# Kernel tuning notes

Measured on AMD Instinct MI355X. Metric: run time of the kernel, lower is better.

Reference implementation:

```python
import math
import jax, jax.numpy as jnp
import numpy as np

SEQ_LEN = 512
NUM_HEADS = 16
HEAD_DIM = 64  # hidden_size // num_heads
MAX_REL = 127


def _relative_positions_embeddings(length, depth, max_relative_position=MAX_REL):
    """Sinusoidal table gathered by clipped relative distance -> [L, L, depth]."""
    vocab = 2 * max_relative_position + 1
    pos = np.arange(vocab, dtype=np.float64)[:, None]
    i = np.arange(depth // 2, dtype=np.float64)[None, :]
    angle = pos / np.power(10000.0, 2.0 * i / depth)
    table = np.zeros((vocab, depth), dtype=np.float64)
    table[:, 0::2] = np.sin(angle)
    table[:, 1::2] = np.cos(angle)
    r = np.arange(length)
    dist = np.clip(r[None, :] - r[:, None], -max_relative_position, max_relative_position)
    final = dist + max_relative_position  # [L, L] indices into vocab
    return jnp.asarray(table[final], dtype=jnp.float32)  # [L, L, depth]

_REL_EMB = _relative_positions_embeddings(SEQ_LEN, HEAD_DIM)


def setup_inputs() -> dict:
    key = jax.random.key(0)
    ks = jax.random.split(key, 4)
    B, S, H = 8, SEQ_LEN, NUM_HEADS * HEAD_DIM
    scale = 1.0 / math.sqrt(H)
    return {
        "hidden_states": jax.random.normal(ks[0], (B, S, H), dtype=jnp.float32),
        "attention_mask": jnp.zeros((B, 1, 1, S), dtype=jnp.float32),
        "Wq": jax.random.normal(ks[1], (H, H), dtype=jnp.float32) * scale,
        "bq": jnp.zeros((H,), dtype=jnp.float32),
        "Wk": jax.random.normal(ks[2], (H, H), dtype=jnp.float32) * scale,
        "bk": jnp.zeros((H,), dtype=jnp.float32),
        "Wv": jax.random.normal(ks[3], (H, H), dtype=jnp.float32) * scale,
        "bv": jnp.zeros((H,), dtype=jnp.float32),
    }


def reference(hidden_states, attention_mask, Wq, bq, Wk, bk, Wv, bv):
    B, S, _ = hidden_states.shape
    H, D = NUM_HEADS, HEAD_DIM

    def split_heads(x):  # [B,S,H*D] -> [B,H,S,D]
        return x.reshape(B, S, H, D).transpose(0, 2, 1, 3)

    q = split_heads(hidden_states @ Wq.T + bq)
    k = split_heads(hidden_states @ Wk.T + bk)
    v = split_heads(hidden_states @ Wv.T + bv)

    rel = _REL_EMB[:S, :S, :]  # [S, S, D]

    scores = jnp.einsum("bhqd,bhkd->bhqk", q, k)
    scores = scores + jnp.einsum("bhqd,qkd->bhqk", q, rel)
    scores = scores / math.sqrt(D) + attention_mask

    probs = jax.nn.softmax(scores, axis=-1)  # dropout prob = 0.0 (eval)

    ctx = jnp.einsum("bhqk,bhkd->bhqd", probs, v)
    ctx = ctx + jnp.einsum("bhqk,qkd->bhqd", probs, rel)

    context_layer = ctx.transpose(0, 2, 1, 3).reshape(B, S, H * D)
    return context_layer, scores
```

## Files before the change

kernel.cpp:

```cpp
#include <hip/hip_runtime.h>
#include <hip/hip_bf16.h>

typedef __attribute__((ext_vector_type(4))) float f32x4;
typedef __attribute__((ext_vector_type(8))) short bf16x8;

#define NB 8
#define NS 512
#define NH 16
#define ND 64
#define HID 1024
#define NBH (NB*NH)
#define NROWS (NB*NS)

static __device__ __forceinline__ ushort f2bf(float x){
    union{float f; unsigned u;} a; a.f = x;
    unsigned r = a.u + 0x7fffu + ((a.u >> 16) & 1u);
    return (ushort)(r >> 16);
}
static __device__ __forceinline__ float bf2f(ushort x){
    union{unsigned u; float f;} a; a.u = ((unsigned)x) << 16;
    return a.f;
}

__global__ void build_tables(ushort* __restrict__ tab, ushort* __restrict__ tabT){
    int t = blockIdx.x * blockDim.x + threadIdx.x;
    if (t >= 256 * 64) return;
    int p = t >> 6, d = t & 63;
    float val = 0.f;
    if (p < 255){
        int i = d >> 1;
        float angle = (float)p / powf(10000.f, (float)i / 32.f);
        val = (d & 1) ? cosf(angle) : sinf(angle);
    }
    ushort b = f2bf(val);
    tab[p * 64 + d]  = b;
    tabT[d * 256 + p] = b;
}

__global__ void cvt_bf16(const float* __restrict__ src, ushort* __restrict__ dst, int n4){
    int i = blockIdx.x * blockDim.x + threadIdx.x;
    if (i >= n4) return;
    float4 v = reinterpret_cast<const float4*>(src)[i];
    ushort4 o;
    o.x = f2bf(v.x); o.y = f2bf(v.y); o.z = f2bf(v.z); o.w = f2bf(v.w);
    reinterpret_cast<ushort4*>(dst)[i] = o;
}

__global__ void cvt_bf16_w3(const float* __restrict__ w0, const float* __restrict__ w1,
                            const float* __restrict__ w2, ushort* __restrict__ o0,
                            ushort* __restrict__ o1, ushort* __restrict__ o2, int n4){
    int i = blockIdx.x * blockDim.x + threadIdx.x;
    if (i >= n4) return;
    const float* src = blockIdx.y == 0 ? w0 : (blockIdx.y == 1 ? w1 : w2);
    ushort* dst      = blockIdx.y == 0 ? o0 : (blockIdx.y == 1 ? o1 : o2);
    float4 v = reinterpret_cast<const float4*>(src)[i];
    ushort4 o;
    o.x = f2bf(v.x); o.y = f2bf(v.y); o.z = f2bf(v.z); o.w = f2bf(v.w);
    reinterpret_cast<ushort4*>(dst)[i] = o;
}

__global__ __launch_bounds__(256) void proj_gemm_qkv(
    const ushort* __restrict__ X,
    const ushort* __restrict__ Wqp, const ushort* __restrict__ Wkp, const ushort* __restrict__ Wvp,
    const float* __restrict__ bqp, const float* __restrict__ bkp, const float* __restrict__ bvp,
    ushort* __restrict__ outQ, ushort* __restrict__ outK, ushort* __restrict__ outV)
{
    __shared__ ushort lA[128][72];
    __shared__ ushort lB[128][72];
    int sel = blockIdx.x >> 3;
    const ushort* W   = sel == 0 ? Wqp : (sel == 1 ? Wkp : Wvp);
    const float* bias = sel == 0 ? bqp : (sel == 1 ? bkp : bvp);
    ushort* out       = sel == 0 ? outQ : (sel == 1 ? outK : outV);
    int n0 = (blockIdx.x & 7) * 128;
    int m0 = blockIdx.y * 128;
    int tid = threadIdx.x;
    int wave = tid >> 6, lane = tid & 63;
    int wr = (wave >> 1) * 64, wc = (wave & 1) * 64;
    int lrow = lane & 15, lk8 = (lane >> 4) * 8;

    f32x4 acc[4][4] = {};

    for (int k0 = 0; k0 < HID; k0 += 64){
        __syncthreads();
        #pragma unroll
        for (int i = 0; i < 4; ++i){
            int chunk = i * 256 + tid;
            int row = chunk >> 3, col = (chunk & 7) * 8;
            *reinterpret_cast<uint4*>(&lA[row][col]) =
                *reinterpret_cast<const uint4*>(&X[(size_t)(m0 + row) * HID + k0 + col]);
            *reinterpret_cast<uint4*>(&lB[row][col]) =
                *reinterpret_cast<const uint4*>(&W[(size_t)(n0 + row) * HID + k0 + col]);
        }
        __syncthreads();
        #pragma unroll
        for (int ks = 0; ks < 2; ++ks){
            bf16x8 af[4], bfr[4];
            #pragma unroll
            for (int m = 0; m < 4; ++m)
                af[m] = *reinterpret_cast<const bf16x8*>(&lA[wr + m*16 + lrow][ks*32 + lk8]);
            #pragma unroll
            for (int n = 0; n < 4; ++n)
                bfr[n] = *reinterpret_cast<const bf16x8*>(&lB[wc + n*16 + lrow][ks*32 + lk8]);
            #pragma unroll
            for (int m = 0; m < 4; ++m)
                #pragma unroll
                for (int n = 0; n < 4; ++n)
                    acc[m][n] = __builtin_amdgcn_mfma_f32_16x16x32_bf16(af[m], bfr[n], acc[m][n], 0, 0, 0);
        }
    }

    #pragma unroll
    for (int m = 0; m < 4; ++m){
        #pragma unroll
        for (int n = 0; n < 4; ++n){
            int col = n0 + wc + n*16 + lrow;
            float bv = bias[col];
            int h = col >> 6, d = col & 63;
            #pragma unroll
            for (int r = 0; r < 4; ++r){
                int mg = m0 + wr + m*16 + (lane >> 4)*4 + r;
                int b = mg >> 9, s = mg & 511;
                float val = acc[m][n][r] + bv;
                if (sel != 2)
                    out[(((size_t)(b*NH + h))*NS + s)*ND + d] = f2bf(val);
                else
                    out[(((size_t)(b*NH + h))*ND + d)*NS + s] = f2bf(val);
            }
        }
    }
}

__global__ __launch_bounds__(256) void fused_attn(
    const ushort* __restrict__ Qb, const ushort* __restrict__ Kb,
    const ushort* __restrict__ vT, const ushort* __restrict__ tab,
    const ushort* __restrict__ tabT, const float* __restrict__ mask,
    float* __restrict__ scores, float* __restrict__ ctx)
{
    __shared__ ushort pL[16][512];
    __shared__ ushort qq[16][256];
    __shared__ float  rsum[16][4];
    __shared__ float  rleft[16][4];
    __shared__ float  rright[16][4];
    ushort* pLf = &pL[0][0];
    ushort* qqf = &qq[0][0];
#define SWZ(row, col) ((col) ^ (((row)&7)<<3))

    const int bh = blockIdx.x;
    const int b = bh >> 4, h = bh & 15;
    const int q0 = blockIdx.y * 16;
    const int wave = threadIdx.x >> 6, lane = threadIdx.x & 63;
    const int lrow = lane & 15, g = lane >> 4, lk8 = g * 8;

    const ushort* Qh = Qb + (size_t)bh * NS * ND;
    const ushort* Kh = Kb + (size_t)bh * NS * ND;
    const int d = wave*16 + lrow;
    const ushort* vTh = vT + ((size_t)bh*ND + d)*NS;

    bf16x8 qf[2];
    #pragma unroll
    for (int ks = 0; ks < 2; ++ks)
        qf[ks] = *reinterpret_cast<const bf16x8*>(&Qh[(size_t)(q0 + lrow)*ND + ks*32 + lk8]);

    f32x4 acc[12];
    #pragma unroll
    for (int n = 0; n < 12; ++n) acc[n] = (f32x4){0.f, 0.f, 0.f, 0.f};

    #pragma unroll
    for (int n = 0; n < 12; ++n){
        const ushort* src = (n < 8) ? &Kh[(size_t)(wave*128 + n*16 + lrow)*ND]
                                    : &tab[(size_t)(wave*64 + (n-8)*16 + lrow)*ND];
        #pragma unroll
        for (int ks = 0; ks < 2; ++ks){
            bf16x8 kf = *reinterpret_cast<const bf16x8*>(&src[ks*32 + lk8]);
            acc[n] = __builtin_amdgcn_mfma_f32_16x16x32_bf16(kf, qf[ks], acc[n], 0, 0, 0);
        }
    }

    bf16x8 vpre[8];
    #pragma unroll
    for (int i = 0; i < 8; ++i)
        vpre[i] = *reinterpret_cast<const bf16x8*>(&vTh[i*64 + lk8]);

    #pragma unroll
    for (int n = 8; n < 12; ++n){
        ushort4 w;
        w.x = f2bf(acc[n][0]); w.y = f2bf(acc[n][1]);
        w.z = f2bf(acc[n][2]); w.w = f2bf(acc[n][3]);
        int col = wave*64 + (n-8)*16 + g*4;
        *reinterpret_cast<ushort4*>(&qqf[lrow*256 + SWZ(lrow, col)]) = w;
    }
    __syncthreads();

    const int q = q0 + lrow;
    float st = 0.f, sl = 0.f, sr = 0.f;
    #pragma unroll
    for (int n = 0; n < 8; ++n){
        int kbase = wave*128 + n*16 + g*4;
        float4 mk4 = *reinterpret_cast<const float4*>(&mask[b*NS + kbase]);
        float mk[4] = {mk4.x, mk4.y, mk4.z, mk4.w};
        f32x4 sv;
        #pragma unroll
        for (int r = 0; r < 4; ++r){
            int k = kbase + r;
            int dd = min(127, max(-127, k - q));
            float val = (acc[n][r] + bf2f(qqf[lrow*256 + SWZ(lrow, dd + 127)])) * 0.125f + mk[r];
            sv[r] = val;
            float e = __expf(val);
            acc[n][r] = e;
            st += e;
            if (k <= q - 127) sl += e;
            if (k >= q + 127) sr += e;
        }
        __builtin_nontemporal_store(sv,
            reinterpret_cast<f32x4*>(&scores[((size_t)bh*NS + q)*NS + kbase]));
    }
    st += __shfl_xor(st, 16); st += __shfl_xor(st, 32);
    sl += __shfl_xor(sl, 16); sl += __shfl_xor(sl, 32);
    sr += __shfl_xor(sr, 16); sr += __shfl_xor(sr, 32);
    if (lane < 16){
        rsum[lrow][wave] = st;
        rleft[lrow][wave] = sl;
        rright[lrow][wave] = sr;
    }
    __syncthreads();

    float T  = rsum[lrow][0] + rsum[lrow][1] + rsum[lrow][2] + rsum[lrow][3];
    float iv = 1.f / T;
    float Lv = (rleft[lrow][0] + rleft[lrow][1] + rleft[lrow][2] + rleft[lrow][3]) * iv;
    float Rv = (rright[lrow][0] + rright[lrow][1] + rright[lrow][2] + rright[lrow][3]) * iv;

    #pragma unroll
    for (int n = 0; n < 8; ++n){
        int kbase = wave*128 + n*16 + g*4;
        ushort4 w;
        w.x = f2bf(acc[n][0] * iv); w.y = f2bf(acc[n][1] * iv);
        w.z = f2bf(acc[n][2] * iv); w.w = f2bf(acc[n][3] * iv);
        *reinterpret_cast<ushort4*>(&pLf[lrow*512 + SWZ(lrow, kbase)]) = w;
    }
    if (wave == 0 && lane < 16){
        qqf[lrow*256 + SWZ(lrow, 0)]   = f2bf(Lv);
        qqf[lrow*256 + SWZ(lrow, 254)] = f2bf(Rv);
    }
    __syncthreads();

    for (int idx = threadIdx.x; idx < 16*256; idx += 256){
        int row = idx >> 8, j = idx & 255;
        if (j == 0 || j >= 254) continue;
        int col = q0 + row + j - 127;
        qqf[row*256 + SWZ(row, j)] =
            (col >= 0 && col < NS) ? pLf[row*512 + SWZ(row, col)] : (ushort)0;
    }
    __syncthreads();

    const ushort* tTd = tabT + (size_t)d*256;
    f32x4 o0 = (f32x4){0.f,0.f,0.f,0.f};
    f32x4 o1 = (f32x4){0.f,0.f,0.f,0.f};
    #pragma unroll
    for (int i = 0; i < 8; ++i){
        int k0 = i*64;
        bf16x8 pa0 = *reinterpret_cast<const bf16x8*>(&pLf[lrow*512 + SWZ(lrow, k0 + lk8)]);
        o0 = __builtin_amdgcn_mfma_f32_16x16x32_bf16(pa0, vpre[i], o0, 0, 0, 0);
        bf16x8 bv1 = *reinterpret_cast<const bf16x8*>(&vTh[k0 + 32 + lk8]);
        bf16x8 pa1 = *reinterpret_cast<const bf16x8*>(&pLf[lrow*512 + SWZ(lrow, k0 + 32 + lk8)]);
        o1 = __builtin_amdgcn_mfma_f32_16x16x32_bf16(pa1, bv1, o1, 0, 0, 0);
    }
    #pragma unroll
    for (int k0 = 0; k0 < 256; k0 += 64){
        bf16x8 bv0 = *reinterpret_cast<const bf16x8*>(&tTd[k0 + lk8]);
        bf16x8 pa0 = *reinterpret_cast<const bf16x8*>(&qqf[lrow*256 + SWZ(lrow, k0 + lk8)]);
        o0 = __builtin_amdgcn_mfma_f32_16x16x32_bf16(pa0, bv0, o0, 0, 0, 0);
        bf16x8 bv1 = *reinterpret_cast<const bf16x8*>(&tTd[k0 + 32 + lk8]);
        bf16x8 pa1 = *reinterpret_cast<const bf16x8*>(&qqf[lrow*256 + SWZ(lrow, k0 + 32 + lk8)]);
        o1 = __builtin_amdgcn_mfma_f32_16x16x32_bf16(pa1, bv1, o1, 0, 0, 0);
    }
    #pragma unroll
    for (int r = 0; r < 4; ++r){
        int qo = q0 + g*4 + r;
        __builtin_nontemporal_store(o0[r] + o1[r],
            &ctx[((size_t)b*NS + qo)*HID + h*ND + d]);
    }
#undef SWZ
}

extern "C" void kernel_launch(void* const* d_in, const int* in_sizes, int n_in,
                              void* d_out, int out_size, void* d_ws, size_t ws_size,
                              hipStream_t stream)
{
    const float* x    = (const float*)d_in[0];
    const float* mask = (const float*)d_in[1];
    const float* Wq   = (const float*)d_in[2];
    const float* bq   = (const float*)d_in[3];
    const float* Wk   = (const float*)d_in[4];
    const float* bk   = (const float*)d_in[5];
    const float* Wv   = (const float*)d_in[6];
    const float* bv   = (const float*)d_in[7];

    float* out = (float*)d_out;
    float* ctx    = out;
    float* scores = out + (size_t)NB*NS*HID;

    char* ws = (char*)d_ws;
    ushort* x_bf  = (ushort*)ws;  ws += (size_t)NROWS*HID*2;
    ushort* wq_bf = (ushort*)ws;  ws += (size_t)HID*HID*2;
    ushort* wk_bf = (ushort*)ws;  ws += (size_t)HID*HID*2;
    ushort* wv_bf = (ushort*)ws;  ws += (size_t)HID*HID*2;
    ushort* q_bf  = (ushort*)ws;  ws += (size_t)NBH*NS*ND*2;
    ushort* k_bf  = (ushort*)ws;  ws += (size_t)NBH*NS*ND*2;
    ushort* vT_bf = (ushort*)ws;  ws += (size_t)NBH*NS*ND*2;
    ushort* tab   = (ushort*)ws;  ws += 256*64*2;
    ushort* tabT  = (ushort*)ws;  ws += 64*256*2;

    build_tables<<<64, 256, 0, stream>>>(tab, tabT);

    cvt_bf16<<<(NROWS*HID/4 + 255)/256, 256, 0, stream>>>(x, x_bf, NROWS*HID/4);
    cvt_bf16_w3<<<dim3((HID*HID/4 + 255)/256, 3), 256, 0, stream>>>(
        Wq, Wk, Wv, wq_bf, wk_bf, wv_bf, HID*HID/4);

    proj_gemm_qkv<<<dim3(24, 32), 256, 0, stream>>>(
        x_bf, wq_bf, wk_bf, wv_bf, bq, bk, bv, q_bf, k_bf, vT_bf);

    fused_attn<<<dim3(NBH, NS/16), 256, 0, stream>>>(
        q_bf, k_bf, vT_bf, tab, tabT, mask, scores, ctx);
}
```

Measured before the change: 180.2 us.

## Cut register pressure in fused attention by streaming K and deferring normalization

The fused attention kernel no longer keeps all twelve score accumulators and eight prefetched V fragments live. Instead it computes each QK tile on the fly, writes unnormalized bf16 exponentials straight to LDS, and applies the 1/sum softmax scale to the output context at the end. This removes one normalization pass and one barrier, and adds a 6-waves-per-EU launch bound plus s_setprio around the MFMA loop, all aimed at higher occupancy and less latency. In exchange, V loads are no longer prefetched, and unnormalized exponentials rounded to bf16 may change precision slightly.

```diff
diff --git a/kernel.cpp b/kernel.cpp
--- a/kernel.cpp
+++ b/kernel.cpp
@@ -130,7 +130,7 @@
     }
 }
 
-__global__ __launch_bounds__(256) void fused_attn(
+__global__ __launch_bounds__(256, 6) void fused_attn(
     const ushort* __restrict__ Qb, const ushort* __restrict__ Kb,
     const ushort* __restrict__ vT, const ushort* __restrict__ tab,
     const ushort* __restrict__ tabT, const float* __restrict__ mask,
@@ -153,96 +153,71 @@
 
     const ushort* Qh = Qb + (size_t)bh * NS * ND;
     const ushort* Kh = Kb + (size_t)bh * NS * ND;
-    const int d = wave*16 + lrow;
-    const ushort* vTh = vT + ((size_t)bh*ND + d)*NS;
-
-    bf16x8 qf[2];
-    #pragma unroll
-    for (int ks = 0; ks < 2; ++ks)
-        qf[ks] = *reinterpret_cast<const bf16x8*>(&Qh[(size_t)(q0 + lrow)*ND + ks*32 + lk8]);
-
-    f32x4 acc[12];
-    #pragma unroll
-    for (int n = 0; n < 12; ++n) acc[n] = (f32x4){0.f, 0.f, 0.f, 0.f};
-
-    #pragma unroll
-    for (int n = 0; n < 12; ++n){
-        const ushort* src = (n < 8) ? &Kh[(size_t)(wave*128 + n*16 + lrow)*ND]
-                                    : &tab[(size_t)(wave*64 + (n-8)*16 + lrow)*ND];
-        #pragma unroll
-        for (int ks = 0; ks < 2; ++ks){
-            bf16x8 kf = *reinterpret_cast<const bf16x8*>(&src[ks*32 + lk8]);
-            acc[n] = __builtin_amdgcn_mfma_f32_16x16x32_bf16(kf, qf[ks], acc[n], 0, 0, 0);
-        }
-    }
-
-    bf16x8 vpre[8];
-    #pragma unroll
-    for (int i = 0; i < 8; ++i)
-        vpre[i] = *reinterpret_cast<const bf16x8*>(&vTh[i*64 + lk8]);
-
-    #pragma unroll
-    for (int n = 8; n < 12; ++n){
+    const int q = q0 + lrow;
+
+    bf16x8 qf0 = *reinterpret_cast<const bf16x8*>(&Qh[(size_t)(q0 + lrow)*ND + lk8]);
+    bf16x8 qf1 = *reinterpret_cast<const bf16x8*>(&Qh[(size_t)(q0 + lrow)*ND + 32 + lk8]);
+
+    #pragma unroll
+    for (int t = 0; t < 4; ++t){
+        const ushort* src = &tab[(size_t)(wave*64 + t*16 + lrow)*ND];
+        bf16x8 k0v = *reinterpret_cast<const bf16x8*>(&src[lk8]);
+        bf16x8 k1v = *reinterpret_cast<const bf16x8*>(&src[32 + lk8]);
+        f32x4 at = __builtin_amdgcn_mfma_f32_16x16x32_bf16(k0v, qf0, (f32x4){0.f,0.f,0.f,0.f}, 0, 0, 0);
+        at = __builtin_amdgcn_mfma_f32_16x16x32_bf16(k1v, qf1, at, 0, 0, 0);
         ushort4 w;
-        w.x = f2bf(acc[n][0]); w.y = f2bf(acc[n][1]);
-        w.z = f2bf(acc[n][2]); w.w = f2bf(acc[n][3]);
-        int col = wave*64 + (n-8)*16 + g*4;
+        w.x = f2bf(at[0]); w.y = f2bf(at[1]); w.z = f2bf(at[2]); w.w = f2bf(at[3]);
+        int col = wave*64 + t*16 + g*4;
         *reinterpret_cast<ushort4*>(&qqf[lrow*256 + SWZ(lrow, col)]) = w;
     }
     __syncthreads();
 
-    const int q = q0 + lrow;
     float st = 0.f, sl = 0.f, sr = 0.f;
+    const float* maskb = &mask[b*NS];
+    float* srow = &scores[((size_t)bh*NS + q)*NS];
     #pragma unroll
     for (int n = 0; n < 8; ++n){
         int kbase = wave*128 + n*16 + g*4;
-        float4 mk4 = *reinterpret_cast<const float4*>(&mask[b*NS + kbase]);
+        const ushort* src = &Kh[(size_t)(wave*128 + n*16 + lrow)*ND];
+        bf16x8 k0v = *reinterpret_cast<const bf16x8*>(&src[lk8]);
+        bf16x8 k1v = *reinterpret_cast<const bf16x8*>(&src[32 + lk8]);
+        f32x4 a = __builtin_amdgcn_mfma_f32_16x16x32_bf16(k0v, qf0, (f32x4){0.f,0.f,0.f,0.f}, 0, 0, 0);
+        a = __builtin_amdgcn_mfma_f32_16x16x32_bf16(k1v, qf1, a, 0, 0, 0);
+        float4 mk4 = *reinterpret_cast<const float4*>(&maskb[kbase]);
         float mk[4] = {mk4.x, mk4.y, mk4.z, mk4.w};
         f32x4 sv;
+        ushort4 pw;
         #pragma unroll
         for (int r = 0; r < 4; ++r){
             int k = kbase + r;
             int dd = min(127, max(-127, k - q));
-            float val = (acc[n][r] + bf2f(qqf[lrow*256 + SWZ(lrow, dd + 127)])) * 0.125f + mk[r];
+            float val = (a[r] + bf2f(qqf[lrow*256 + SWZ(lrow, dd + 127)])) * 0.125f + mk[r];
             sv[r] = val;
             float e = __expf(val);
-            acc[n][r] = e;
             st += e;
             if (k <= q - 127) sl += e;
             if (k >= q + 127) sr += e;
+            ((ushort*)&pw)[r] = f2bf(e);
         }
-        __builtin_nontemporal_store(sv,
-            reinterpret_cast<f32x4*>(&scores[((size_t)bh*NS + q)*NS + kbase]));
+        __builtin_nontemporal_store(sv, reinterpret_cast<f32x4*>(&srow[kbase]));
+        *reinterpret_cast<ushort4*>(&pLf[lrow*512 + SWZ(lrow, kbase)]) = pw;
     }
     st += __shfl_xor(st, 16); st += __shfl_xor(st, 32);
     sl += __shfl_xor(sl, 16); sl += __shfl_xor(sl, 32);
     sr += __shfl_xor(sr, 16); sr += __shfl_xor(sr, 32);
     if (lane < 16){
-        rsum[lrow][wave] = st;
-        rleft[lrow][wave] = sl;
+        rsum[lrow][wave]   = st;
+        rleft[lrow][wave]  = sl;
         rright[lrow][wave] = sr;
     }
     __syncthreads();
 
-    float T  = rsum[lrow][0] + rsum[lrow][1] + rsum[lrow][2] + rsum[lrow][3];
-    float iv = 1.f / T;
-    float Lv = (rleft[lrow][0] + rleft[lrow][1] + rleft[lrow][2] + rleft[lrow][3]) * iv;
-    float Rv = (rright[lrow][0] + rright[lrow][1] + rright[lrow][2] + rright[lrow][3]) * iv;
-
-    #pragma unroll
-    for (int n = 0; n < 8; ++n){
-        int kbase = wave*128 + n*16 + g*4;
-        ushort4 w;
-        w.x = f2bf(acc[n][0] * iv); w.y = f2bf(acc[n][1] * iv);
-        w.z = f2bf(acc[n][2] * iv); w.w = f2bf(acc[n][3] * iv);
-        *reinterpret_cast<ushort4*>(&pLf[lrow*512 + SWZ(lrow, kbase)]) = w;
-    }
     if (wave == 0 && lane < 16){
-        qqf[lrow*256 + SWZ(lrow, 0)]   = f2bf(Lv);
-        qqf[lrow*256 + SWZ(lrow, 254)] = f2bf(Rv);
-    }
-    __syncthreads();
-
+        float SL = rleft[lrow][0] + rleft[lrow][1] + rleft[lrow][2] + rleft[lrow][3];
+        float SR = rright[lrow][0] + rright[lrow][1] + rright[lrow][2] + rright[lrow][3];
+        qqf[lrow*256 + SWZ(lrow, 0)]   = f2bf(SL);
+        qqf[lrow*256 + SWZ(lrow, 254)] = f2bf(SR);
+    }
     for (int idx = threadIdx.x; idx < 16*256; idx += 256){
         int row = idx >> 8, j = idx & 255;
         if (j == 0 || j >= 254) continue;
@@ -252,14 +227,17 @@
     }
     __syncthreads();
 
+    const int d = wave*16 + lrow;
+    const ushort* vTh = vT + ((size_t)bh*ND + d)*NS;
     const ushort* tTd = tabT + (size_t)d*256;
     f32x4 o0 = (f32x4){0.f,0.f,0.f,0.f};
     f32x4 o1 = (f32x4){0.f,0.f,0.f,0.f};
-    #pragma unroll
-    for (int i = 0; i < 8; ++i){
-        int k0 = i*64;
+    __builtin_amdgcn_s_setprio(1);
+    #pragma unroll
+    for (int k0 = 0; k0 < NS; k0 += 64){
+        bf16x8 bv0 = *reinterpret_cast<const bf16x8*>(&vTh[k0 + lk8]);
         bf16x8 pa0 = *reinterpret_cast<const bf16x8*>(&pLf[lrow*512 + SWZ(lrow, k0 + lk8)]);
-        o0 = __builtin_amdgcn_mfma_f32_16x16x32_bf16(pa0, vpre[i], o0, 0, 0, 0);
+        o0 = __builtin_amdgcn_mfma_f32_16x16x32_bf16(pa0, bv0, o0, 0, 0, 0);
         bf16x8 bv1 = *reinterpret_cast<const bf16x8*>(&vTh[k0 + 32 + lk8]);
         bf16x8 pa1 = *reinterpret_cast<const bf16x8*>(&pLf[lrow*512 + SWZ(lrow, k0 + 32 + lk8)]);
         o1 = __builtin_amdgcn_mfma_f32_16x16x32_bf16(pa1, bv1, o1, 0, 0, 0);
@@ -273,11 +251,13 @@
         bf16x8 pa1 = *reinterpret_cast<const bf16x8*>(&qqf[lrow*256 + SWZ(lrow, k0 + 32 + lk8)]);
         o1 = __builtin_amdgcn_mfma_f32_16x16x32_bf16(pa1, bv1, o1, 0, 0, 0);
     }
+    __builtin_amdgcn_s_setprio(0);
     #pragma unroll
     for (int r = 0; r < 4; ++r){
-        int qo = q0 + g*4 + r;
-        __builtin_nontemporal_store(o0[r] + o1[r],
-            &ctx[((size_t)b*NS + qo)*HID + h*ND + d]);
+        int row = g*4 + r;
+        float T = rsum[row][0] + rsum[row][1] + rsum[row][2] + rsum[row][3];
+        int qo = q0 + row;
+        ctx[((size_t)b*NS + qo)*HID + h*ND + d] = (o0[r] + o1[r]) * (1.f / T);
     }
 #undef SWZ
 }
```

Result: faster. 175.7 us (-2.5%).
